# Performance work log

Measured on AMD Instinct MI355X. Metric: run time of the kernel, lower is better.

## Reference

```python
import math
import jax, jax.numpy as jnp
import numpy as np

H, PQ, PV = 12, 8, 12
C_S = 384
INF, EPS = 1e5, 1e-8
SOFTPLUS_INV_1 = 0.541324854612918


def _rand_rot(key, shape):
    """Random rotation matrices via normalized quaternions, shape + (3,3)."""
    q = jax.random.normal(key, shape + (4,))
    q = q / jnp.linalg.norm(q, axis=-1, keepdims=True)
    w, x, y, z = q[..., 0], q[..., 1], q[..., 2], q[..., 3]
    R = jnp.stack([
        1 - 2 * (y * y + z * z), 2 * (x * y - w * z), 2 * (x * z + w * y),
        2 * (x * y + w * z), 1 - 2 * (x * x + z * z), 2 * (y * z - w * x),
        2 * (x * z - w * y), 2 * (y * z + w * x), 1 - 2 * (x * x + y * y),
    ], axis=-1).reshape(shape + (3, 3))
    return R


def setup_inputs() -> dict:
    key = jax.random.key(0)
    ks = jax.random.split(key, 12)
    B, N1, N2 = 2, 2048, 512
    s1 = jax.random.normal(ks[0], (B, N1, C_S), dtype=jnp.float32)
    s2 = jax.random.normal(ks[1], (B, N2, C_S), dtype=jnp.float32)
    r1_rot = _rand_rot(ks[2], (B, N1)).astype(jnp.float32)
    r2_rot = _rand_rot(ks[3], (B, N2)).astype(jnp.float32)
    r1_trans = jax.random.normal(ks[4], (B, N1, 3), dtype=jnp.float32)
    r2_trans = jax.random.normal(ks[5], (B, N2, 3), dtype=jnp.float32)
    mask1 = jnp.ones((B, N1), dtype=jnp.float32)
    mask2 = jnp.ones((B, N2), dtype=jnp.float32)
    Wq = jax.random.normal(ks[6], (C_S, H * PQ * 3), dtype=jnp.float32) / math.sqrt(C_S)
    Wkv = jax.random.normal(ks[7], (C_S, H * (PQ + PV) * 3), dtype=jnp.float32) / math.sqrt(C_S)
    head_weights = jnp.full((H,), SOFTPLUS_INV_1, dtype=jnp.float32)
    Wout = jax.random.normal(ks[8], (H * PV * 4, C_S), dtype=jnp.float32) * 0.02
    bout = jnp.zeros((C_S,), dtype=jnp.float32)
    return {"s1": s1, "s2": s2, "r1_rot": r1_rot, "r1_trans": r1_trans,
            "r2_rot": r2_rot, "r2_trans": r2_trans, "mask1": mask1, "mask2": mask2,
            "Wq": Wq, "Wkv": Wkv, "head_weights": head_weights,
            "Wout": Wout, "bout": bout}


def reference(s1, s2, r1_rot, r1_trans, r2_rot, r2_trans, mask1, mask2,
              Wq, Wkv, head_weights, Wout, bout):
    B, N1, _ = s1.shape
    N2 = s2.shape[1]

    # query points: linear -> [B,N1,3,H,PQ] (torch split/stack layout) -> local [B,N1,H,PQ,3]
    q = jnp.moveaxis((s1 @ Wq).reshape(B, N1, 3, H, PQ), 2, -1)
    # rigid apply: R x + t (global frame)
    q = jnp.einsum('bimn,bihpn->bihpm', r1_rot, q) + r1_trans[:, :, None, None, :]

    kv = jnp.moveaxis((s2 @ Wkv).reshape(B, N2, 3, H, PQ + PV), 2, -1)
    kv = jnp.einsum('bjmn,bjhpn->bjhpm', r2_rot, kv) + r2_trans[:, :, None, None, :]
    k, v = kv[..., :PQ, :], kv[..., PQ:, :]  # [B,N2,H,PQ,3], [B,N2,H,PV,3]

    # sum_p ||q_p - k_p||^2 via norm expansion (avoids [B,N1,N2,H,PQ,3] tensor)
    qn = jnp.sum(q * q, axis=(-1, -2))                     # [B,N1,H]
    kn = jnp.sum(k * k, axis=(-1, -2))                     # [B,N2,H]
    cross = jnp.einsum('bihpc,bjhpc->bijh', q, k)          # [B,N1,N2,H]
    d2 = qn[:, :, None, :] + kn[:, None, :, :] - 2.0 * cross

    hw = jax.nn.softplus(head_weights) * math.sqrt(1.0 / (3 * (PQ * 9.0 / 2)))
    att = jnp.transpose(-0.5 * d2 * hw, (0, 3, 1, 2))      # [B,H,N1,N2]
    bias = INF * (mask1[:, :, None] * mask2[:, None, :] - 1.0)
    a = jax.nn.softmax(att + bias[:, None], axis=-1)

    o = jnp.einsum('bhij,bjhpc->bihpc', a, v)              # [B,N1,H,PV,3]
    # rigid invert_apply: R^T (x - t), back into local frame of residue i
    o_loc = jnp.einsum('bimn,bihpm->bihpn', r1_rot, o - r1_trans[:, :, None, None, :])

    dists = jnp.sqrt(jnp.sum(o_loc * o_loc, axis=-1) + EPS)   # [B,N1,H,PV]
    o_flat = o_loc.reshape(B, N1, H * PV, 3)
    feats = jnp.concatenate([o_flat[..., 0], o_flat[..., 1], o_flat[..., 2],
                             dists.reshape(B, N1, H * PV)], axis=-1)
    return feats @ Wout + bout
```

## Files before the change

kernel.cpp:

```cpp
#include <hip/hip_runtime.h>
#include <math.h>

#define B_ 2
#define N1_ 2048
#define N2_ 512
#define CS_ 384
#define H_ 12
#define PQ_ 8
#define PV_ 12
#define PKV_ 20
#define CQ_ (H_*PQ_*3)
#define CKV_ (H_*PKV_*3)
#define INF_ 100000.0f
#define HW_SCALE_ 0.09622504486493764f

typedef __attribute__((ext_vector_type(8))) short bf16x8;
typedef __attribute__((ext_vector_type(4))) float f32x4;

__device__ inline unsigned short f2bf(float x) {
  unsigned u = __float_as_uint(x);
  u += 0x7fffu + ((u >> 16) & 1u);
  return (unsigned short)(u >> 16);
}

__device__ inline bf16x8 cvt8(const float* __restrict__ p) {
  float4 a = *(const float4*)p;
  float4 b = *(const float4*)(p + 4);
  bf16x8 r;
  r[0] = (short)f2bf(a.x); r[1] = (short)f2bf(a.y);
  r[2] = (short)f2bf(a.z); r[3] = (short)f2bf(a.w);
  r[4] = (short)f2bf(b.x); r[5] = (short)f2bf(b.y);
  r[6] = (short)f2bf(b.z); r[7] = (short)f2bf(b.w);
  return r;
}

#define TQ_   108
#define TKV_  276
#define TWO_  216
#define VPAD_ 72
#define KN_   12
__global__ __launch_bounds__(256) void prep_kernel(
    const float* __restrict__ Wq, const float* __restrict__ Wkv,
    const float* __restrict__ Wout,
    unsigned short* __restrict__ wqT, unsigned short* __restrict__ wkvT,
    unsigned short* __restrict__ woutT,
    unsigned short* __restrict__ vtb, float* __restrict__ kn)
{
  __shared__ float lds[32][33];
  int blk = blockIdx.x, t = threadIdx.x;
  int rr0 = t >> 5, cc = t & 31;

  const float* src = nullptr; unsigned short* dst = nullptr;
  int K = 0, N = 0, k0 = 0, n0 = 0;
  if (blk < TQ_) {
    src = Wq; dst = wqT; K = 384; N = CQ_;
    k0 = (blk % 12) * 32; n0 = (blk / 12) * 32;
  } else if (blk < TQ_ + TKV_) {
    int b2 = blk - TQ_;
    src = Wkv; dst = wkvT; K = 384; N = CKV_;
    k0 = (b2 % 12) * 32; n0 = (b2 / 12) * 32;
  } else if (blk < TQ_ + TKV_ + TWO_) {
    int b3 = blk - TQ_ - TKV_;
    src = Wout; dst = woutT; K = 576; N = CS_;
    k0 = (b3 % 18) * 32; n0 = (b3 / 18) * 32;
  } else if (blk < TQ_ + TKV_ + TWO_ + VPAD_) {
    int idx = (blk - TQ_ - TKV_ - TWO_)*256 + t;
    int f = idx * 8;
    int run = f >> 9, off = f & 511;
    int bh = run / 12, cc2 = 36 + run % 12;
    uint4 z = {0u,0u,0u,0u};
    *(uint4*)(vtb + ((size_t)bh*48 + cc2)*512 + off) = z;
    return;
  } else {
    int idx = (blk - TQ_ - TKV_ - TWO_ - VPAD_)*256 + t;
    float4 z = {0.f,0.f,0.f,0.f};
    *(float4*)(kn + (size_t)idx*4) = z;
    return;
  }

  #pragma unroll
  for (int rr = 0; rr < 4; ++rr) {
    int r = rr0 + rr*8;
    if (n0 + cc < N) lds[r][cc] = src[(size_t)(k0 + r)*N + n0 + cc];
  }
  __syncthreads();
  #pragma unroll
  for (int rr = 0; rr < 4; ++rr) {
    int r = rr0 + rr*8;
    if (n0 + r < N) dst[(size_t)(n0 + r)*K + k0 + cc] = f2bf(lds[cc][r]);
  }
}

__global__ __launch_bounds__(256) void qproj_mfma(
    const float* __restrict__ s1, const unsigned short* __restrict__ wqT,
    const float* __restrict__ rot, const float* __restrict__ trans,
    unsigned short* __restrict__ qgb, float* __restrict__ qn)
{
  int wave = threadIdx.x >> 6, lane = threadIdx.x & 63;
  int col = lane & 15, g = lane >> 4;
  int wg = blockIdx.x*4 + wave;
  int strip = wg / 6;
  int nt = wg % 6;
  int i0 = strip * 16;

  f32x4 ax = {0.f,0.f,0.f,0.f}, ay = ax, az = ax;
  const float* arow = s1 + (size_t)(i0 + col)*CS_;
  const unsigned short* bx = wqT + (size_t)((nt     )*16 + col)*CS_;
  const unsigned short* by = wqT + (size_t)((nt +  6)*16 + col)*CS_;
  const unsigned short* bz = wqT + (size_t)((nt + 12)*16 + col)*CS_;
  #pragma unroll
  for (int k = 0; k < CS_; k += 32) {
    bf16x8 a = cvt8(arow + k + g*8);
    ax = __builtin_amdgcn_mfma_f32_16x16x32_bf16(a, *(const bf16x8*)(bx + k + g*8), ax, 0,0,0);
    ay = __builtin_amdgcn_mfma_f32_16x16x32_bf16(a, *(const bf16x8*)(by + k + g*8), ay, 0,0,0);
    az = __builtin_amdgcn_mfma_f32_16x16x32_bf16(a, *(const bf16x8*)(bz + k + g*8), az, 0,0,0);
  }

  int p = nt*16 + col;
  int h = p >> 3, pq = p & 7;
  float qsum[4];
  #pragma unroll
  for (int r = 0; r < 4; ++r) {
    int row = i0 + g*4 + r;
    const float* R  = rot   + (size_t)row*9;
    const float* tr = trans + (size_t)row*3;
    float x = ax[r], y = ay[r], z = az[r];
    float g0 = R[0]*x + R[1]*y + R[2]*z + tr[0];
    float g1 = R[3]*x + R[4]*y + R[5]*z + tr[1];
    float g2 = R[6]*x + R[7]*y + R[8]*z + tr[2];
    int b = row >> 11, i = row & (N1_-1);
    size_t rbase = ((size_t)(b*H_ + h)*N1_ + i)*32;
    qgb[rbase + pq*3]     = f2bf(g0);
    qgb[rbase + pq*3 + 1] = f2bf(g1);
    qgb[rbase + pq*3 + 2] = f2bf(g2);
    if (pq == 7) {
      uint4 z4 = {0u,0u,0u,0u};
      *(uint4*)(qgb + rbase + 24) = z4;
    }
    qsum[r] = g0*g0 + g1*g1 + g2*g2;
  }
  #pragma unroll
  for (int r = 0; r < 4; ++r) {
    qsum[r] += __shfl_xor(qsum[r], 1);
    qsum[r] += __shfl_xor(qsum[r], 2);
    qsum[r] += __shfl_xor(qsum[r], 4);
  }
  if ((col & 7) == 0) {
    int hh = nt*2 + (col >> 3);
    #pragma unroll
    for (int r = 0; r < 4; ++r) {
      int row = i0 + g*4 + r;
      int b = row >> 11, i = row & (N1_-1);
      qn[(size_t)(b*H_ + hh)*N1_ + i] = qsum[r];
    }
  }
}

__global__ __launch_bounds__(256) void kvproj_mfma(
    const float* __restrict__ s2, const unsigned short* __restrict__ wkvT,
    const float* __restrict__ rot, const float* __restrict__ trans,
    unsigned short* __restrict__ kgb, unsigned short* __restrict__ vtb,
    float* __restrict__ kn)
{
  int wave = threadIdx.x >> 6, lane = threadIdx.x & 63;
  int col = lane & 15, g = lane >> 4;
  int wg = blockIdx.x*4 + wave;
  int strip = wg / 15;
  int nt = wg % 15;
  int row0 = strip * 16;

  f32x4 ax = {0.f,0.f,0.f,0.f}, ay = ax, az = ax;
  const float* arow = s2 + (size_t)(row0 + col)*CS_;
  const unsigned short* bx = wkvT + (size_t)(nt*16       + col)*CS_;
  const unsigned short* by = wkvT + (size_t)(nt*16 + 240 + col)*CS_;
  const unsigned short* bz = wkvT + (size_t)(nt*16 + 480 + col)*CS_;
  #pragma unroll
  for (int k = 0; k < CS_; k += 32) {
    bf16x8 a = cvt8(arow + k + g*8);
    ax = __builtin_amdgcn_mfma_f32_16x16x32_bf16(a, *(const bf16x8*)(bx + k + g*8), ax, 0,0,0);
    ay = __builtin_amdgcn_mfma_f32_16x16x32_bf16(a, *(const bf16x8*)(by + k + g*8), ay, 0,0,0);
    az = __builtin_amdgcn_mfma_f32_16x16x32_bf16(a, *(const bf16x8*)(bz + k + g*8), az, 0,0,0);
  }

  int p = nt*16 + col;
  int h = p / PKV_, pp = p % PKV_;
  #pragma unroll
  for (int r = 0; r < 4; ++r) {
    int row = row0 + g*4 + r;
    const float* R  = rot   + (size_t)row*9;
    const float* tr = trans + (size_t)row*3;
    float x = ax[r], y = ay[r], z = az[r];
    float g0 = R[0]*x + R[1]*y + R[2]*z + tr[0];
    float g1 = R[3]*x + R[4]*y + R[5]*z + tr[1];
    float g2 = R[6]*x + R[7]*y + R[8]*z + tr[2];
    int b = row >> 9, j = row & (N2_-1);
    int bh = b*H_ + h;
    if (pp < PQ_) {
      size_t base = ((size_t)bh*N2_ + j)*32 + pp*3;
      kgb[base]   = f2bf(g0);
      kgb[base+1] = f2bf(g1);
      kgb[base+2] = f2bf(g2);
      if (pp == 0) {
        uint4 z4 = {0u,0u,0u,0u};
        *(uint4*)(kgb + ((size_t)bh*N2_ + j)*32 + 24) = z4;
      }
      atomicAdd(&kn[(size_t)bh*N2_ + j], g0*g0 + g1*g1 + g2*g2);
    } else {
      int comp = (pp - PQ_)*3;
      size_t base = ((size_t)bh*48 + comp)*512 + j;
      vtb[base]        = f2bf(g0);
      vtb[base + 512]  = f2bf(g1);
      vtb[base + 1024] = f2bf(g2);
    }
  }
}

#define RSTRIDE 72
#define OSTRIDE 52
__global__ __launch_bounds__(256) void attn_kernel(
    const unsigned short* __restrict__ qgb, const float* __restrict__ qn,
    const unsigned short* __restrict__ kgb, const unsigned short* __restrict__ vtb,
    const float* __restrict__ kn, const float* __restrict__ mask1,
    const float* __restrict__ mask2, const float* __restrict__ hwts,
    const float* __restrict__ rot, const float* __restrict__ trans,
    unsigned short* __restrict__ featsb)
{
  __shared__ __align__(16) unsigned short pstrip[4][16][RSTRIDE];
  __shared__ float o_s[4][16][OSTRIDE];
  __shared__ float l_s[4][16];

  int wave = threadIdx.x >> 6;
  int lane = threadIdx.x & 63;
  int col = lane & 15, g = lane >> 4;
  int mt = blockIdx.x*4 + wave;
  int bh = mt >> 7;
  int it = mt & 127;
  int b = bh / H_, h = bh - b*H_;

  float hw = logf(1.0f + __expf(hwts[h])) * HW_SCALE_;

  bf16x8 qa = *(const bf16x8*)(qgb + (((size_t)bh*N1_ + it*16 + col)*32 + g*8));

  float ar[4], m1r[4];
  #pragma unroll
  for (int r = 0; r < 4; ++r) {
    int ig = it*16 + g*4 + r;
    ar[r]  = fmaf(-0.5f*hw, qn[(size_t)bh*N1_ + ig], -INF_);
    m1r[r] = mask1[b*N1_ + ig] * INF_;
  }

  f32x4 ot[3];
  #pragma unroll
  for (int m = 0; m < 3; ++m) ot[m] = (f32x4){0.f,0.f,0.f,0.f};
  float l[4] = {0.f,0.f,0.f,0.f};

  const unsigned short* kbase = kgb + (size_t)bh*N2_*32;
  const unsigned short* vbase = vtb + (size_t)bh*48*512;
  const float* knp = kn + (size_t)bh*N2_;
  const float* m2p = mask2 + b*N2_;

  for (int jt = 0; jt < 8; ++jt) {
    int j0 = jt*64;
    #pragma unroll
    for (int nt = 0; nt < 4; ++nt) {
      int jg = j0 + nt*16 + col;
      bf16x8 kb = *(const bf16x8*)(kbase + ((size_t)jg*32 + g*8));
      f32x4 dotv = __builtin_amdgcn_mfma_f32_16x16x32_bf16(
          qa, kb, (f32x4){0.f,0.f,0.f,0.f}, 0, 0, 0);
      float bc  = -0.5f*hw*knp[jg];
      float m2c = m2p[jg];
      #pragma unroll
      for (int r = 0; r < 4; ++r) {
        float logit = fmaf(hw, dotv[r], fmaf(m1r[r], m2c, ar[r] + bc));
        float w = __expf(logit);
        l[r] += w;
        pstrip[wave][g*4 + r][nt*16 + col] = f2bf(w);
      }
    }
    #pragma unroll
    for (int ks = 0; ks < 2; ++ks) {
      bf16x8 pb = *(const bf16x8*)&pstrip[wave][col][ks*32 + g*8];
      #pragma unroll
      for (int mtv = 0; mtv < 3; ++mtv) {
        bf16x8 va = *(const bf16x8*)(vbase +
            ((size_t)(mtv*16 + col))*512 + j0 + ks*32 + g*8);
        ot[mtv] = __builtin_amdgcn_mfma_f32_16x16x32_bf16(va, pb, ot[mtv], 0, 0, 0);
      }
    }
  }

  #pragma unroll
  for (int r = 0; r < 4; ++r) {
    l[r] += __shfl_xor(l[r], 1);
    l[r] += __shfl_xor(l[r], 2);
    l[r] += __shfl_xor(l[r], 4);
    l[r] += __shfl_xor(l[r], 8);
  }
  if (col == 0) {
    #pragma unroll
    for (int r = 0; r < 4; ++r) l_s[wave][g*4 + r] = l[r];
  }
  #pragma unroll
  for (int mtv = 0; mtv < 3; ++mtv)
    #pragma unroll
    for (int r = 0; r < 4; ++r)
      o_s[wave][col][mtv*16 + g*4 + r] = ot[mtv][r];
  __syncthreads();

  float inv = 1.0f / l_s[wave][col];
  int ig = it*16 + col;
  int row = b*N1_ + ig;
  const float* R  = rot   + (size_t)row*9;
  const float* tr = trans + (size_t)row*3;
  float R00=R[0],R01=R[1],R02=R[2],R10=R[3],R11=R[4],R12=R[5],R20=R[6],R21=R[7],R22=R[8];
  float t0=tr[0], t1=tr[1], t2=tr[2];
  unsigned short* fb = featsb + (size_t)row*576 + h*PV_;
  #pragma unroll
  for (int p = 0; p < 3; ++p) {
    int pt = g*3 + p;
    float ox = o_s[wave][col][pt*3+0]*inv - t0;
    float oy = o_s[wave][col][pt*3+1]*inv - t1;
    float oz = o_s[wave][col][pt*3+2]*inv - t2;
    float lx = R00*ox + R10*oy + R20*oz;
    float ly = R01*ox + R11*oy + R21*oz;
    float lz = R02*ox + R12*oy + R22*oz;
    float dist = sqrtf(lx*lx + ly*ly + lz*lz + 1e-8f);
    fb[pt]       = f2bf(lx);
    fb[144 + pt] = f2bf(ly);
    fb[288 + pt] = f2bf(lz);
    fb[432 + pt] = f2bf(dist);
  }
}

__global__ __launch_bounds__(512) void outproj_mfma(
    const unsigned short* __restrict__ featsb, const unsigned short* __restrict__ woutT,
    const float* __restrict__ bout, float* __restrict__ out)
{
  int wave = threadIdx.x >> 6, lane = threadIdx.x & 63;
  int col = lane & 15, g = lane >> 4;
  int i0 = blockIdx.x * 16;
  int n0 = wave * 48;

  f32x4 acc[3];
  #pragma unroll
  for (int m = 0; m < 3; ++m) acc[m] = (f32x4){0.f,0.f,0.f,0.f};
  const unsigned short* arow = featsb + (size_t)(i0 + col)*576;
  const unsigned short* b0 = woutT + (size_t)(n0      + col)*576;
  const unsigned short* b1 = woutT + (size_t)(n0 + 16 + col)*576;
  const unsigned short* b2 = woutT + (size_t)(n0 + 32 + col)*576;
  #pragma unroll 3
  for (int k = 0; k < 576; k += 32) {
    bf16x8 a = *(const bf16x8*)(arow + k + g*8);
    acc[0] = __builtin_amdgcn_mfma_f32_16x16x32_bf16(a, *(const bf16x8*)(b0 + k + g*8), acc[0], 0,0,0);
    acc[1] = __builtin_amdgcn_mfma_f32_16x16x32_bf16(a, *(const bf16x8*)(b1 + k + g*8), acc[1], 0,0,0);
    acc[2] = __builtin_amdgcn_mfma_f32_16x16x32_bf16(a, *(const bf16x8*)(b2 + k + g*8), acc[2], 0,0,0);
  }
  #pragma unroll
  for (int t3 = 0; t3 < 3; ++t3) {
    int n = n0 + t3*16 + col;
    float bb = bout[n];
    #pragma unroll
    for (int r = 0; r < 4; ++r) {
      int row = i0 + g*4 + r;
      out[(size_t)row*CS_ + n] = acc[t3][r] + bb;
    }
  }
}

extern "C" void kernel_launch(void* const* d_in, const int* in_sizes, int n_in,
                              void* d_out, int out_size, void* d_ws, size_t ws_size,
                              hipStream_t stream) {
  const float* s1       = (const float*)d_in[0];
  const float* s2       = (const float*)d_in[1];
  const float* r1_rot   = (const float*)d_in[2];
  const float* r1_trans = (const float*)d_in[3];
  const float* r2_rot   = (const float*)d_in[4];
  const float* r2_trans = (const float*)d_in[5];
  const float* mask1    = (const float*)d_in[6];
  const float* mask2    = (const float*)d_in[7];
  const float* Wq       = (const float*)d_in[8];
  const float* Wkv      = (const float*)d_in[9];
  const float* hwts     = (const float*)d_in[10];
  const float* Wout     = (const float*)d_in[11];
  const float* bout     = (const float*)d_in[12];
  float* out = (float*)d_out;

  float* qn = (float*)d_ws;
  float* kn = qn + (size_t)B_*H_*N1_;
  unsigned short* featsb = (unsigned short*)(kn + (size_t)B_*H_*N2_);
  unsigned short* qgb  = featsb + (size_t)B_*N1_*576;
  unsigned short* kgb  = qgb  + (size_t)B_*H_*N1_*32;
  unsigned short* vtb  = kgb  + (size_t)B_*H_*N2_*32;
  unsigned short* wqT  = vtb  + (size_t)B_*H_*48*512;
  unsigned short* wkvT = wqT  + (size_t)CQ_*CS_;
  unsigned short* woutT= wkvT + (size_t)CKV_*CS_;

  prep_kernel<<<TQ_+TKV_+TWO_+VPAD_+KN_, 256, 0, stream>>>(
      Wq, Wkv, Wout, wqT, wkvT, woutT, vtb, kn);
  qproj_mfma<<<384, 256, 0, stream>>>(s1, wqT, r1_rot, r1_trans, qgb, qn);
  kvproj_mfma<<<240, 256, 0, stream>>>(s2, wkvT, r2_rot, r2_trans, kgb, vtb, kn);
  attn_kernel<<<(B_*H_*(N1_/16))/4, 256, 0, stream>>>(qgb, qn, kgb, vtb, kn, mask1, mask2,
                                                      hwts, r1_rot, r1_trans, featsb);
  outproj_mfma<<<256, 512, 0, stream>>>(featsb, woutT, bout, out);
}
```

Measured before the change: 162.6 us.

## Merge projection kernels and split attention and out-projection reductions across waves

Fuses the Q and KV projection kernels into a single launch dispatched by block index, saving one launch. The attention kernel now splits the N2 key range between pairs of waves and combines partial sums and denominators through shared memory, doubling the number of blocks. The output projection splits K across two wave groups with an LDS reduction. Together these raise parallelism and occupancy for a small problem, at the cost of extra shared-memory traffic and idle waves in the epilogues.

```diff
diff --git a/kernel.cpp b/kernel.cpp
--- a/kernel.cpp
+++ b/kernel.cpp
@@ -91,126 +91,124 @@
   }
 }
 
-__global__ __launch_bounds__(256) void qproj_mfma(
-    const float* __restrict__ s1, const unsigned short* __restrict__ wqT,
-    const float* __restrict__ rot, const float* __restrict__ trans,
-    unsigned short* __restrict__ qgb, float* __restrict__ qn)
-{
-  int wave = threadIdx.x >> 6, lane = threadIdx.x & 63;
-  int col = lane & 15, g = lane >> 4;
-  int wg = blockIdx.x*4 + wave;
-  int strip = wg / 6;
-  int nt = wg % 6;
-  int i0 = strip * 16;
-
-  f32x4 ax = {0.f,0.f,0.f,0.f}, ay = ax, az = ax;
-  const float* arow = s1 + (size_t)(i0 + col)*CS_;
-  const unsigned short* bx = wqT + (size_t)((nt     )*16 + col)*CS_;
-  const unsigned short* by = wqT + (size_t)((nt +  6)*16 + col)*CS_;
-  const unsigned short* bz = wqT + (size_t)((nt + 12)*16 + col)*CS_;
-  #pragma unroll
-  for (int k = 0; k < CS_; k += 32) {
-    bf16x8 a = cvt8(arow + k + g*8);
-    ax = __builtin_amdgcn_mfma_f32_16x16x32_bf16(a, *(const bf16x8*)(bx + k + g*8), ax, 0,0,0);
-    ay = __builtin_amdgcn_mfma_f32_16x16x32_bf16(a, *(const bf16x8*)(by + k + g*8), ay, 0,0,0);
-    az = __builtin_amdgcn_mfma_f32_16x16x32_bf16(a, *(const bf16x8*)(bz + k + g*8), az, 0,0,0);
-  }
-
-  int p = nt*16 + col;
-  int h = p >> 3, pq = p & 7;
-  float qsum[4];
-  #pragma unroll
-  for (int r = 0; r < 4; ++r) {
-    int row = i0 + g*4 + r;
-    const float* R  = rot   + (size_t)row*9;
-    const float* tr = trans + (size_t)row*3;
-    float x = ax[r], y = ay[r], z = az[r];
-    float g0 = R[0]*x + R[1]*y + R[2]*z + tr[0];
-    float g1 = R[3]*x + R[4]*y + R[5]*z + tr[1];
-    float g2 = R[6]*x + R[7]*y + R[8]*z + tr[2];
-    int b = row >> 11, i = row & (N1_-1);
-    size_t rbase = ((size_t)(b*H_ + h)*N1_ + i)*32;
-    qgb[rbase + pq*3]     = f2bf(g0);
-    qgb[rbase + pq*3 + 1] = f2bf(g1);
-    qgb[rbase + pq*3 + 2] = f2bf(g2);
-    if (pq == 7) {
-      uint4 z4 = {0u,0u,0u,0u};
-      *(uint4*)(qgb + rbase + 24) = z4;
-    }
-    qsum[r] = g0*g0 + g1*g1 + g2*g2;
-  }
-  #pragma unroll
-  for (int r = 0; r < 4; ++r) {
-    qsum[r] += __shfl_xor(qsum[r], 1);
-    qsum[r] += __shfl_xor(qsum[r], 2);
-    qsum[r] += __shfl_xor(qsum[r], 4);
-  }
-  if ((col & 7) == 0) {
-    int hh = nt*2 + (col >> 3);
-    #pragma unroll
-    for (int r = 0; r < 4; ++r) {
-      int row = i0 + g*4 + r;
-      int b = row >> 11, i = row & (N1_-1);
-      qn[(size_t)(b*H_ + hh)*N1_ + i] = qsum[r];
-    }
-  }
-}
-
-__global__ __launch_bounds__(256) void kvproj_mfma(
-    const float* __restrict__ s2, const unsigned short* __restrict__ wkvT,
-    const float* __restrict__ rot, const float* __restrict__ trans,
+__global__ __launch_bounds__(256) void proj_mfma(
+    const float* __restrict__ s1, const float* __restrict__ s2,
+    const unsigned short* __restrict__ wqT, const unsigned short* __restrict__ wkvT,
+    const float* __restrict__ r1_rot, const float* __restrict__ r1_trans,
+    const float* __restrict__ r2_rot, const float* __restrict__ r2_trans,
+    unsigned short* __restrict__ qgb, float* __restrict__ qn,
     unsigned short* __restrict__ kgb, unsigned short* __restrict__ vtb,
     float* __restrict__ kn)
 {
   int wave = threadIdx.x >> 6, lane = threadIdx.x & 63;
   int col = lane & 15, g = lane >> 4;
-  int wg = blockIdx.x*4 + wave;
-  int strip = wg / 15;
-  int nt = wg % 15;
-  int row0 = strip * 16;
-
-  f32x4 ax = {0.f,0.f,0.f,0.f}, ay = ax, az = ax;
-  const float* arow = s2 + (size_t)(row0 + col)*CS_;
-  const unsigned short* bx = wkvT + (size_t)(nt*16       + col)*CS_;
-  const unsigned short* by = wkvT + (size_t)(nt*16 + 240 + col)*CS_;
-  const unsigned short* bz = wkvT + (size_t)(nt*16 + 480 + col)*CS_;
-  #pragma unroll
-  for (int k = 0; k < CS_; k += 32) {
-    bf16x8 a = cvt8(arow + k + g*8);
-    ax = __builtin_amdgcn_mfma_f32_16x16x32_bf16(a, *(const bf16x8*)(bx + k + g*8), ax, 0,0,0);
-    ay = __builtin_amdgcn_mfma_f32_16x16x32_bf16(a, *(const bf16x8*)(by + k + g*8), ay, 0,0,0);
-    az = __builtin_amdgcn_mfma_f32_16x16x32_bf16(a, *(const bf16x8*)(bz + k + g*8), az, 0,0,0);
-  }
-
-  int p = nt*16 + col;
-  int h = p / PKV_, pp = p % PKV_;
-  #pragma unroll
-  for (int r = 0; r < 4; ++r) {
-    int row = row0 + g*4 + r;
-    const float* R  = rot   + (size_t)row*9;
-    const float* tr = trans + (size_t)row*3;
-    float x = ax[r], y = ay[r], z = az[r];
-    float g0 = R[0]*x + R[1]*y + R[2]*z + tr[0];
-    float g1 = R[3]*x + R[4]*y + R[5]*z + tr[1];
-    float g2 = R[6]*x + R[7]*y + R[8]*z + tr[2];
-    int b = row >> 9, j = row & (N2_-1);
-    int bh = b*H_ + h;
-    if (pp < PQ_) {
-      size_t base = ((size_t)bh*N2_ + j)*32 + pp*3;
-      kgb[base]   = f2bf(g0);
-      kgb[base+1] = f2bf(g1);
-      kgb[base+2] = f2bf(g2);
-      if (pp == 0) {
+
+  if (blockIdx.x < 384) {
+    int wg = blockIdx.x*4 + wave;
+    int strip = wg / 6;
+    int nt = wg % 6;
+    int i0 = strip * 16;
+
+    f32x4 ax = {0.f,0.f,0.f,0.f}, ay = ax, az = ax;
+    const float* arow = s1 + (size_t)(i0 + col)*CS_;
+    const unsigned short* bx = wqT + (size_t)((nt     )*16 + col)*CS_;
+    const unsigned short* by = wqT + (size_t)((nt +  6)*16 + col)*CS_;
+    const unsigned short* bz = wqT + (size_t)((nt + 12)*16 + col)*CS_;
+    #pragma unroll
+    for (int k = 0; k < CS_; k += 32) {
+      bf16x8 a = cvt8(arow + k + g*8);
+      ax = __builtin_amdgcn_mfma_f32_16x16x32_bf16(a, *(const bf16x8*)(bx + k + g*8), ax, 0,0,0);
+      ay = __builtin_amdgcn_mfma_f32_16x16x32_bf16(a, *(const bf16x8*)(by + k + g*8), ay, 0,0,0);
+      az = __builtin_amdgcn_mfma_f32_16x16x32_bf16(a, *(const bf16x8*)(bz + k + g*8), az, 0,0,0);
+    }
+
+    int p = nt*16 + col;
+    int h = p >> 3, pq = p & 7;
+    float qsum[4];
+    #pragma unroll
+    for (int r = 0; r < 4; ++r) {
+      int row = i0 + g*4 + r;
+      const float* R  = r1_rot   + (size_t)row*9;
+      const float* tr = r1_trans + (size_t)row*3;
+      float x = ax[r], y = ay[r], z = az[r];
+      float g0 = R[0]*x + R[1]*y + R[2]*z + tr[0];
+      float g1 = R[3]*x + R[4]*y + R[5]*z + tr[1];
+      float g2 = R[6]*x + R[7]*y + R[8]*z + tr[2];
+      int b = row >> 11, i = row & (N1_-1);
+      size_t rbase = ((size_t)(b*H_ + h)*N1_ + i)*32;
+      qgb[rbase + pq*3]     = f2bf(g0);
+      qgb[rbase + pq*3 + 1] = f2bf(g1);
+      qgb[rbase + pq*3 + 2] = f2bf(g2);
+      if (pq == 7) {
         uint4 z4 = {0u,0u,0u,0u};
-        *(uint4*)(kgb + ((size_t)bh*N2_ + j)*32 + 24) = z4;
+        *(uint4*)(qgb + rbase + 24) = z4;
       }
-      atomicAdd(&kn[(size_t)bh*N2_ + j], g0*g0 + g1*g1 + g2*g2);
-    } else {
-      int comp = (pp - PQ_)*3;
-      size_t base = ((size_t)bh*48 + comp)*512 + j;
-      vtb[base]        = f2bf(g0);
-      vtb[base + 512]  = f2bf(g1);
-      vtb[base + 1024] = f2bf(g2);
+      qsum[r] = g0*g0 + g1*g1 + g2*g2;
+    }
+    #pragma unroll
+    for (int r = 0; r < 4; ++r) {
+      qsum[r] += __shfl_xor(qsum[r], 1);
+      qsum[r] += __shfl_xor(qsum[r], 2);
+      qsum[r] += __shfl_xor(qsum[r], 4);
+    }
+    if ((col & 7) == 0) {
+      int hh = nt*2 + (col >> 3);
+      #pragma unroll
+      for (int r = 0; r < 4; ++r) {
+        int row = i0 + g*4 + r;
+        int b = row >> 11, i = row & (N1_-1);
+        qn[(size_t)(b*H_ + hh)*N1_ + i] = qsum[r];
+      }
+    }
+  } else {
+    int wg = (blockIdx.x - 384)*4 + wave;
+    int strip = wg / 15;
+    int nt = wg % 15;
+    int row0 = strip * 16;
+
+    f32x4 ax = {0.f,0.f,0.f,0.f}, ay = ax, az = ax;
+    const float* arow = s2 + (size_t)(row0 + col)*CS_;
+    const unsigned short* bx = wkvT + (size_t)(nt*16       + col)*CS_;
+    const unsigned short* by = wkvT + (size_t)(nt*16 + 240 + col)*CS_;
+    const unsigned short* bz = wkvT + (size_t)(nt*16 + 480 + col)*CS_;
+    #pragma unroll
+    for (int k = 0; k < CS_; k += 32) {
+      bf16x8 a = cvt8(arow + k + g*8);
+      ax = __builtin_amdgcn_mfma_f32_16x16x32_bf16(a, *(const bf16x8*)(bx + k + g*8), ax, 0,0,0);
+      ay = __builtin_amdgcn_mfma_f32_16x16x32_bf16(a, *(const bf16x8*)(by + k + g*8), ay, 0,0,0);
+      az = __builtin_amdgcn_mfma_f32_16x16x32_bf16(a, *(const bf16x8*)(bz + k + g*8), az, 0,0,0);
+    }
+
+    int p = nt*16 + col;
+    int h = p / PKV_, pp = p % PKV_;
+    #pragma unroll
+    for (int r = 0; r < 4; ++r) {
+      int row = row0 + g*4 + r;
+      const float* R  = r2_rot   + (size_t)row*9;
+      const float* tr = r2_trans + (size_t)row*3;
+      float x = ax[r], y = ay[r], z = az[r];
+      float g0 = R[0]*x + R[1]*y + R[2]*z + tr[0];
+      float g1 = R[3]*x + R[4]*y + R[5]*z + tr[1];
+      float g2 = R[6]*x + R[7]*y + R[8]*z + tr[2];
+      int b = row >> 9, j = row & (N2_-1);
+      int bh = b*H_ + h;
+      if (pp < PQ_) {
+        size_t base = ((size_t)bh*N2_ + j)*32 + pp*3;
+        kgb[base]   = f2bf(g0);
+        kgb[base+1] = f2bf(g1);
+        kgb[base+2] = f2bf(g2);
+        if (pp == 0) {
+          uint4 z4 = {0u,0u,0u,0u};
+          *(uint4*)(kgb + ((size_t)bh*N2_ + j)*32 + 24) = z4;
+        }
+        atomicAdd(&kn[(size_t)bh*N2_ + j], g0*g0 + g1*g1 + g2*g2);
+      } else {
+        int comp = (pp - PQ_)*3;
+        size_t base = ((size_t)bh*48 + comp)*512 + j;
+        vtb[base]        = f2bf(g0);
+        vtb[base + 512]  = f2bf(g1);
+        vtb[base + 1024] = f2bf(g2);
+      }
     }
   }
 }
@@ -232,7 +230,8 @@
   int wave = threadIdx.x >> 6;
   int lane = threadIdx.x & 63;
   int col = lane & 15, g = lane >> 4;
-  int mt = blockIdx.x*4 + wave;
+  int pair = wave >> 1, half = wave & 1;
+  int mt = blockIdx.x*2 + pair;
   int bh = mt >> 7;
   int it = mt & 127;
   int b = bh / H_, h = bh - b*H_;
@@ -259,7 +258,7 @@
   const float* knp = kn + (size_t)bh*N2_;
   const float* m2p = mask2 + b*N2_;
 
-  for (int jt = 0; jt < 8; ++jt) {
+  for (int jt = half*4; jt < half*4 + 4; ++jt) {
     int j0 = jt*64;
     #pragma unroll
     for (int nt = 0; nt < 4; ++nt) {
@@ -306,8 +305,9 @@
     for (int r = 0; r < 4; ++r)
       o_s[wave][col][mtv*16 + g*4 + r] = ot[mtv][r];
   __syncthreads();
-
-  float inv = 1.0f / l_s[wave][col];
+  if (half) return;
+
+  float inv = 1.0f / (l_s[wave][col] + l_s[wave+1][col]);
   int ig = it*16 + col;
   int row = b*N1_ + ig;
   const float* R  = rot   + (size_t)row*9;
@@ -318,9 +318,9 @@
   #pragma unroll
   for (int p = 0; p < 3; ++p) {
     int pt = g*3 + p;
-    float ox = o_s[wave][col][pt*3+0]*inv - t0;
-    float oy = o_s[wave][col][pt*3+1]*inv - t1;
-    float oz = o_s[wave][col][pt*3+2]*inv - t2;
+    float ox = (o_s[wave][col][pt*3+0] + o_s[wave+1][col][pt*3+0])*inv - t0;
+    float oy = (o_s[wave][col][pt*3+1] + o_s[wave+1][col][pt*3+1])*inv - t1;
+    float oz = (o_s[wave][col][pt*3+2] + o_s[wave+1][col][pt*3+2])*inv - t2;
     float lx = R00*ox + R10*oy + R20*oz;
     float ly = R01*ox + R11*oy + R21*oz;
     float lz = R02*ox + R12*oy + R22*oz;
@@ -332,29 +332,40 @@
   }
 }
 
-__global__ __launch_bounds__(512) void outproj_mfma(
+__global__ __launch_bounds__(1024) void outproj_mfma(
     const unsigned short* __restrict__ featsb, const unsigned short* __restrict__ woutT,
     const float* __restrict__ bout, float* __restrict__ out)
 {
+  __shared__ float acc_s[8][16][48];
   int wave = threadIdx.x >> 6, lane = threadIdx.x & 63;
   int col = lane & 15, g = lane >> 4;
+  int nw = wave & 7, kh = wave >> 3;
   int i0 = blockIdx.x * 16;
-  int n0 = wave * 48;
+  int n0 = nw * 48;
 
   f32x4 acc[3];
   #pragma unroll
   for (int m = 0; m < 3; ++m) acc[m] = (f32x4){0.f,0.f,0.f,0.f};
-  const unsigned short* arow = featsb + (size_t)(i0 + col)*576;
-  const unsigned short* b0 = woutT + (size_t)(n0      + col)*576;
-  const unsigned short* b1 = woutT + (size_t)(n0 + 16 + col)*576;
-  const unsigned short* b2 = woutT + (size_t)(n0 + 32 + col)*576;
+  const unsigned short* arow = featsb + (size_t)(i0 + col)*576 + kh*288;
+  const unsigned short* b0 = woutT + (size_t)(n0      + col)*576 + kh*288;
+  const unsigned short* b1 = woutT + (size_t)(n0 + 16 + col)*576 + kh*288;
+  const unsigned short* b2 = woutT + (size_t)(n0 + 32 + col)*576 + kh*288;
   #pragma unroll 3
-  for (int k = 0; k < 576; k += 32) {
+  for (int k = 0; k < 288; k += 32) {
     bf16x8 a = *(const bf16x8*)(arow + k + g*8);
     acc[0] = __builtin_amdgcn_mfma_f32_16x16x32_bf16(a, *(const bf16x8*)(b0 + k + g*8), acc[0], 0,0,0);
     acc[1] = __builtin_amdgcn_mfma_f32_16x16x32_bf16(a, *(const bf16x8*)(b1 + k + g*8), acc[1], 0,0,0);
     acc[2] = __builtin_amdgcn_mfma_f32_16x16x32_bf16(a, *(const bf16x8*)(b2 + k + g*8), acc[2], 0,0,0);
   }
+  if (kh) {
+    #pragma unroll
+    for (int t3 = 0; t3 < 3; ++t3)
+      #pragma unroll
+      for (int r = 0; r < 4; ++r)
+        acc_s[nw][g*4 + r][t3*16 + col] = acc[t3][r];
+  }
+  __syncthreads();
+  if (kh) return;
   #pragma unroll
   for (int t3 = 0; t3 < 3; ++t3) {
     int n = n0 + t3*16 + col;
@@ -362,7 +373,7 @@
     #pragma unroll
     for (int r = 0; r < 4; ++r) {
       int row = i0 + g*4 + r;
-      out[(size_t)row*CS_ + n] = acc[t3][r] + bb;
+      out[(size_t)row*CS_ + n] = acc[t3][r] + acc_s[nw][g*4 + r][t3*16 + col] + bb;
     }
   }
 }
@@ -397,9 +408,9 @@
 
   prep_kernel<<<TQ_+TKV_+TWO_+VPAD_+KN_, 256, 0, stream>>>(
       Wq, Wkv, Wout, wqT, wkvT, woutT, vtb, kn);
-  qproj_mfma<<<384, 256, 0, stream>>>(s1, wqT, r1_rot, r1_trans, qgb, qn);
-  kvproj_mfma<<<240, 256, 0, stream>>>(s2, wkvT, r2_rot, r2_trans, kgb, vtb, kn);
-  attn_kernel<<<(B_*H_*(N1_/16))/4, 256, 0, stream>>>(qgb, qn, kgb, vtb, kn, mask1, mask2,
-                                                      hwts, r1_rot, r1_trans, featsb);
-  outproj_mfma<<<256, 512, 0, stream>>>(featsb, woutT, bout, out);
-}
+  proj_mfma<<<624, 256, 0, stream>>>(s1, s2, wqT, wkvT, r1_rot, r1_trans,
+                                     r2_rot, r2_trans, qgb, qn, kgb, vtb, kn);
+  attn_kernel<<<B_*H_*(N1_/32), 256, 0, stream>>>(qgb, qn, kgb, vtb, kn, mask1, mask2,
+                                                  hwts, r1_rot, r1_trans, featsb);
+  outproj_mfma<<<256, 1024, 0, stream>>>(featsb, woutT, bout, out);
+}
```

After: 158.3 us. 1.03x faster.
